# Optimization experiments

Hardware: AMD Instinct MI355X
Metric: run time of the kernel (lower is better)

Reference implementation:

```python
import jax, jax.numpy as jnp
import numpy as np

Z, Y, X = 200, 8, 200
XM, YM, ZM = 80.0, 6.0, 80.0  # x_meter, y_meter, z_meter
IMG_H, IMG_W = 256, 512
FEAT_C, OUT_CH = 64, 128
EPS = 1e-8


def create_grid3d():
    # matches torch create_grid3d flattening order (z, y, x), x/y shifted by -0.5
    zz, yy, xx = jnp.meshgrid(jnp.linspace(0.0, 1.0, Z),
                              jnp.linspace(0.0, 1.0, Y),
                              jnp.linspace(0.0, 1.0, X), indexing='ij')
    xyz = jnp.stack([xx.ravel() - 0.5, yy.ravel() - 0.5, zz.ravel()], axis=1)  # (N,3)
    return xyz * jnp.array([XM, YM, ZM], dtype=jnp.float32)


def setup_inputs() -> dict:
    key = jax.random.key(0)
    k1, k2, k3 = jax.random.split(key, 3)
    B = 2
    img_feat = jax.random.normal(k1, (B, FEAT_C, 32, 64), dtype=jnp.float32)
    # realistic pinhole intrinsics so many voxels project in-bounds
    K = jnp.array([[300.0, 0.0, IMG_W / 2.0],
                   [0.0, 300.0, IMG_H / 2.0],
                   [0.0, 0.0, 1.0]], dtype=jnp.float32)
    pix_T_cam = jnp.tile(K[None], (B, 1, 1))
    conv_w = jax.random.normal(k2, (OUT_CH, FEAT_C * Y), dtype=jnp.float32) * 0.02
    conv_b = jax.random.normal(k3, (OUT_CH,), dtype=jnp.float32) * 0.02
    return {"img_feat": img_feat, "pix_T_cam": pix_T_cam, "conv_w": conv_w, "conv_b": conv_b}


def reference(img_feat, pix_T_cam, conv_w, conv_b):
    B, C, H, W = img_feat.shape
    xyz = create_grid3d()  # (N,3), N = Z*Y*X
    pix = jnp.einsum('bij,nj->bni', pix_T_cam, xyz)  # (B,N,3)
    d = pix[..., 2]
    u01 = pix[..., 0] / (d + EPS) / IMG_W  # normalized [0,1] u
    v01 = pix[..., 1] / (d + EPS) / IMG_H
    valid = (u01 >= 0) & (v01 >= 0) & (u01 <= 1) & (v01 <= 1)  # (B,N)

    # grid_sample, align_corners=False, padding_mode='zeros' (D=1 collapses to bilinear)
    gx = u01 * 2.0 - 1.0
    gy = v01 * 2.0 - 1.0
    xp = ((gx + 1.0) * W - 1.0) * 0.5
    yp = ((gy + 1.0) * H - 1.0) * 0.5
    x0f = jnp.floor(xp); y0f = jnp.floor(yp)
    wx1 = xp - x0f; wy1 = yp - y0f
    x0 = x0f.astype(jnp.int32); y0 = y0f.astype(jnp.int32)
    bidx = jnp.arange(B)[:, None]

    def gather(xi, yi):
        ok = (xi >= 0) & (xi < W) & (yi >= 0) & (yi < H)
        xc = jnp.clip(xi, 0, W - 1)
        yc = jnp.clip(yi, 0, H - 1)
        vals = img_feat[bidx, :, yc, xc]  # (B,N,C)
        return vals * ok[..., None].astype(img_feat.dtype)

    v00 = gather(x0, y0)
    v01_ = gather(x0 + 1, y0)
    v10 = gather(x0, y0 + 1)
    v11 = gather(x0 + 1, y0 + 1)
    samp = (v00 * ((1 - wx1) * (1 - wy1))[..., None]
            + v01_ * (wx1 * (1 - wy1))[..., None]
            + v10 * ((1 - wx1) * wy1)[..., None]
            + v11 * (wx1 * wy1)[..., None])  # (B,N,C)
    samp = samp * valid[..., None].astype(samp.dtype)

    bev = samp.reshape(B, Z, Y, X, C)
    # rearrange 'b c d h w -> b (c h) d w' with d=Z, h=Y, w=X
    bev = jnp.transpose(bev, (0, 4, 2, 1, 3)).reshape(B, C * Y, Z, X)
    out = jnp.einsum('bczx,oc->bozx', bev, conv_w) + conv_b[None, :, None, None]
    return out
```

## Files before the change

### kernel.cpp

```cpp
#include <hip/hip_runtime.h>


#define NPOS 40000

typedef short bf16x8 __attribute__((ext_vector_type(8)));
typedef float f32x4  __attribute__((ext_vector_type(4)));

__device__ __forceinline__ unsigned rne16(float f) {
    unsigned u = __float_as_uint(f);
    return (u + 0x7fffu + ((u >> 16) & 1u)) >> 16;
}
__device__ __forceinline__ float lo16(unsigned u) { return __uint_as_float(u << 16); }
__device__ __forceinline__ float hi16(unsigned u) { return __uint_as_float(u & 0xffff0000u); }
__device__ __forceinline__ unsigned cvtpk(float lo, float hi) {
    unsigned r;
    asm("v_cvt_pk_bf16_f32 %0, %1, %2" : "=v"(r) : "v"(lo), "v"(hi));
    return r;
}
__device__ __forceinline__ void pkfma(float2& a, float2 v, float2 w) {
    asm("v_pk_fma_f32 %0, %1, %2, %0" : "+v"(a) : "v"(v), "v"(w));
}
__device__ __forceinline__ void tile_barrier() {
    asm volatile("s_waitcnt lgkmcnt(0)" ::: "memory");
    __builtin_amdgcn_s_barrier();
    __builtin_amdgcn_sched_barrier(0);
}

__global__ __launch_bounds__(256)
void bili_prep(const float* __restrict__ img, const float* __restrict__ convw,
               unsigned short* __restrict__ imgT, unsigned short* __restrict__ Wp)
{
    const int t = threadIdx.x;
    if (blockIdx.x < 128) {
        const int u   = blockIdx.x * 256 + t;
        const int li8 = u & 7, x = (u >> 3) & 63, y = (u >> 9) & 31, b = u >> 14;
        const float* src = img + (((b * 64 + li8 * 8) * 32 + y) * 64 + x);
        unsigned pk[4];
        #pragma unroll
        for (int cc = 0; cc < 8; ++cc) {
            const unsigned v = rne16(src[cc * 2048]);
            if ((cc & 1) == 0) pk[cc >> 1] = v;
            else               pk[cc >> 1] |= (v << 16);
        }
        ((uint4*)imgT)[u] = make_uint4(pk[0], pk[1], pk[2], pk[3]);
    } else {
        const int j = (blockIdx.x - 128) * 256 + t;
        const int k = j & 511, o = j >> 9;
        const int y = k >> 6, c = k & 63;
        Wp[j] = (unsigned short)rne16(convw[o * 512 + c * 8 + y]);
    }
}

__global__ __launch_bounds__(256, 3)
void bili_main(const char* __restrict__ imgTbytes,
               const unsigned short* __restrict__ Wp,
               const float* __restrict__ pixT,
               const float* __restrict__ convb,
               float* __restrict__ out)
{
    __shared__ uint4  Fb[2][1024];
    __shared__ uint4  offsB[512];
    __shared__ float4 wtsL[512];

    const int t   = threadIdx.x;
    const int bx  = blockIdx.x;
    const int b   = (bx >= 625) ? 1 : 0;
    const int n0  = (bx - b * 625) * 64;

    const int wv  = t >> 6;
    const int ln  = t & 63;
    const int l15 = ln & 15;
    const int lg  = ln >> 4;
    const int g   = t >> 3;
    const unsigned liOff = (unsigned)((t & 7) << 4);

    f32x4 acc0[4], acc1[4];
    {
        float bias0[4], bias1[4];
        #pragma unroll
        for (int r = 0; r < 4; ++r) {
            bias0[r] = convb[wv * 32 +      lg * 4 + r];
            bias1[r] = convb[wv * 32 + 16 + lg * 4 + r];
        }
        #pragma unroll
        for (int nt = 0; nt < 4; ++nt)
            #pragma unroll
            for (int r = 0; r < 4; ++r) { acc0[nt][r] = bias0[r]; acc1[nt][r] = bias1[r]; }
    }

    {
        const float* Kb = pixT + b * 9;
        const float K00 = Kb[0], K01 = Kb[1], K02 = Kb[2];
        const float K10 = Kb[3], K11 = Kb[4], K12 = Kb[5];
        const float K20 = Kb[6], K21 = Kb[7], K22 = Kb[8];

        #pragma unroll
        for (int r = 0; r < 2; ++r) {
            const int p    = r * 256 + t;
            const int nloc = p >> 3;
            const int y    = p & 7;
            const int n = n0 + nloc;
            const int z = n / 200;
            const int x = n - z * 200;

            const float pxv = (x * (1.0f / 199.0f) - 0.5f) * 80.0f;
            const float pzv = (z * (1.0f / 199.0f)) * 80.0f;
            const float pyv = (y * (1.0f / 7.0f) - 0.5f) * 6.0f;

            const float p0 = K00 * pxv + K01 * pyv + K02 * pzv;
            const float p1 = K10 * pxv + K11 * pyv + K12 * pzv;
            const float d  = K20 * pxv + K21 * pyv + K22 * pzv;
            const float inv = __builtin_amdgcn_rcpf(d + 1e-8f);
            const float u01 = p0 * inv * (1.0f / 512.0f);
            const float v01 = p1 * inv * (1.0f / 256.0f);
            const float vf = (u01 >= 0.0f && u01 <= 1.0f &&
                              v01 >= 0.0f && v01 <= 1.0f) ? 1.0f : 0.0f;

            float xp = u01 * 64.0f - 0.5f;
            xp = fminf(fmaxf(xp, -2.0f), 66.0f);
            const float x0f = floorf(xp);
            const float wx = xp - x0f;
            const int x0 = (int)x0f, x1i = x0 + 1;
            const float wx0 = (1.0f - wx) * vf * ((x0  >= 0 && x0  < 64) ? 1.0f : 0.0f);
            const float wx1 = wx          * vf * ((x1i >= 0 && x1i < 64) ? 1.0f : 0.0f);
            const int xi0 = min(max(x0, 0), 63);
            const int xi1 = min(max(x1i, 0), 63);

            float yp = v01 * 32.0f - 0.5f;
            yp = fminf(fmaxf(yp, -2.0f), 34.0f);
            const float y0f = floorf(yp);
            const float wy = yp - y0f;
            const int y0 = (int)y0f, y1i = y0 + 1;
            const float wy0 = (1.0f - wy) * ((y0  >= 0 && y0  < 32) ? 1.0f : 0.0f);
            const float wy1 = wy          * ((y1i >= 0 && y1i < 32) ? 1.0f : 0.0f);
            const int yi0 = min(max(y0, 0), 31);
            const int yi1 = min(max(y1i, 0), 31);

            const unsigned o0 = (unsigned)(((yi0 << 6) + xi0) << 7);
            const unsigned o1 = (unsigned)(((yi0 << 6) + xi1) << 7);
            const unsigned o2 = (unsigned)(((yi1 << 6) + xi0) << 7);
            const unsigned o3 = (unsigned)(((yi1 << 6) + xi1) << 7);

            wtsL[p]  = make_float4(wx0 * wy0, wx1 * wy0, wx0 * wy1, wx1 * wy1);
            offsB[p] = make_uint4(o0, o1, o2, o3);
        }
    }

    tile_barrier();

    const char*   imgTb = imgTbytes + (size_t)b * 262144;
    const bf16x8* ApG   = (const bf16x8*)Wp;
    const bf16x8* Ap0   = ApG + ((wv * 32 +      l15) * 64 + lg);
    const bf16x8* Ap1   = ApG + ((wv * 32 + 16 + l15) * 64 + lg);

    uint4 sbE[8], sbO[8];

    #define ISSUE_H(q, hb, SB)                                                 \
        _Pragma("unroll")                                                      \
        for (int it2 = 0; it2 < 2; ++it2) {                                    \
            const int pp = ((hb) * 2 + it2) * 32 + g;                          \
            const int n_ = pp >> 1, ys = pp & 1;                               \
            const int p_ = n_ * 8 + 2 * (q) + ys;                              \
            const uint4 oc = offsB[p_];                                        \
            SB[it2 * 4 + 0] = *(const uint4*)(imgTb + (size_t)(oc.x | liOff)); \
            SB[it2 * 4 + 1] = *(const uint4*)(imgTb + (size_t)(oc.y | liOff)); \
            SB[it2 * 4 + 2] = *(const uint4*)(imgTb + (size_t)(oc.z | liOff)); \
            SB[it2 * 4 + 3] = *(const uint4*)(imgTb + (size_t)(oc.w | liOff)); \
        }

    #define PROC_H(q, hb, SB, buf)                                             \
        _Pragma("unroll")                                                      \
        for (int it2 = 0; it2 < 2; ++it2) {                                    \
            const int pp = ((hb) * 2 + it2) * 32 + g;                          \
            const int n_ = pp >> 1, ys = pp & 1;                               \
            const int p_ = n_ * 8 + 2 * (q) + ys;                              \
            const float4 w = wtsL[p_];                                         \
            float2 ac[4];                                                      \
            _Pragma("unroll")                                                  \
            for (int qq = 0; qq < 4; ++qq) ac[qq] = make_float2(0.0f, 0.0f);   \
            _Pragma("unroll")                                                  \
            for (int j = 0; j < 4; ++j) {                                      \
                const uint4 v = SB[it2 * 4 + j];                               \
                const float ww = (j == 0) ? w.x : (j == 1) ? w.y : (j == 2) ? w.z : w.w; \
                const float2 w2 = make_float2(ww, ww);                         \
                float2 t0, t1, t2, t3;                                         \
                t0.x = lo16(v.x); t0.y = hi16(v.x);                            \
                t1.x = lo16(v.y); t1.y = hi16(v.y);                            \
                t2.x = lo16(v.z); t2.y = hi16(v.z);                            \
                t3.x = lo16(v.w); t3.y = hi16(v.w);                            \
                pkfma(ac[0], t0, w2);                                          \
                pkfma(ac[1], t1, w2);                                          \
                pkfma(ac[2], t2, w2);                                          \
                pkfma(ac[3], t3, w2);                                          \
            }                                                                  \
            uint4 pk;                                                          \
            pk.x = cvtpk(ac[0].x, ac[0].y);                                    \
            pk.y = cvtpk(ac[1].x, ac[1].y);                                    \
            pk.z = cvtpk(ac[2].x, ac[2].y);                                    \
            pk.w = cvtpk(ac[3].x, ac[3].y);                                    \
            (buf)[n_ * 16 + ((ys * 8 + (t & 7)) ^ (n_ & 7))] = pk;             \
        }

    #define MFMA_H(q, hf, buf)                                                 \
        do {                                                                   \
            const bf16x8* Fv = (const bf16x8*)(buf);                           \
            __builtin_amdgcn_s_setprio(1);                                     \
            _Pragma("unroll")                                                  \
            for (int k2 = 0; k2 < 2; ++k2) {                                   \
                const int k = (hf) * 2 + k2;                                   \
                const bf16x8 a0_ = Ap0[((q) * 4 + k) * 4];                     \
                const bf16x8 a1_ = Ap1[((q) * 4 + k) * 4];                     \
                _Pragma("unroll")                                              \
                for (int nt = 0; nt < 4; ++nt) {                               \
                    const int nn = nt * 16 + l15;                              \
                    const bf16x8 bv = Fv[nn * 16 + ((k * 4 + lg) ^ (nn & 7))]; \
                    acc0[nt] = __builtin_amdgcn_mfma_f32_16x16x32_bf16(a0_, bv, acc0[nt], 0, 0, 0); \
                    acc1[nt] = __builtin_amdgcn_mfma_f32_16x16x32_bf16(a1_, bv, acc1[nt], 0, 0, 0); \
                }                                                              \
            }                                                                  \
            __builtin_amdgcn_s_setprio(0);                                     \
        } while (0)

    ISSUE_H(0, 0, sbE);
    ISSUE_H(0, 1, sbO);
    PROC_H (0, 0, sbE, Fb[0]);
    ISSUE_H(1, 0, sbE);
    PROC_H (0, 1, sbO, Fb[0]);
    tile_barrier();

    ISSUE_H(1, 1, sbO);
    MFMA_H (0, 0, Fb[0]);
    PROC_H (1, 0, sbE, Fb[1]);
    ISSUE_H(2, 0, sbE);
    MFMA_H (0, 1, Fb[0]);
    PROC_H (1, 1, sbO, Fb[1]);
    tile_barrier();

    ISSUE_H(2, 1, sbO);
    MFMA_H (1, 0, Fb[1]);
    PROC_H (2, 0, sbE, Fb[0]);
    ISSUE_H(3, 0, sbE);
    MFMA_H (1, 1, Fb[1]);
    PROC_H (2, 1, sbO, Fb[0]);
    tile_barrier();

    ISSUE_H(3, 1, sbO);
    MFMA_H (2, 0, Fb[0]);
    PROC_H (3, 0, sbE, Fb[1]);
    MFMA_H (2, 1, Fb[0]);
    PROC_H (3, 1, sbO, Fb[1]);
    tile_barrier();

    MFMA_H (3, 0, Fb[1]);
    MFMA_H (3, 1, Fb[1]);

    #undef ISSUE_H
    #undef PROC_H
    #undef MFMA_H

    {
        float* ob = out + (size_t)(b * 128 + wv * 32) * NPOS + n0;
        #pragma unroll
        for (int nt = 0; nt < 4; ++nt) {
            #pragma unroll
            for (int r = 0; r < 4; ++r) {
                ob[(     lg * 4 + r) * NPOS + nt * 16 + l15] = acc0[nt][r];
                ob[(16 + lg * 4 + r) * NPOS + nt * 16 + l15] = acc1[nt][r];
            }
        }
    }
}

extern "C" void kernel_launch(void* const* d_in, const int* in_sizes, int n_in,
                              void* d_out, int out_size, void* d_ws, size_t ws_size,
                              hipStream_t stream) {
    const float* img   = (const float*)d_in[0];
    const float* pixT  = (const float*)d_in[1];
    const float* convw = (const float*)d_in[2];
    const float* convb = (const float*)d_in[3];
    float* out = (float*)d_out;

    unsigned short* imgT = (unsigned short*)d_ws;
    unsigned short* Wp   = imgT + 262144;

    hipLaunchKernelGGL(bili_prep, dim3(384), dim3(256), 0, stream,
                       img, convw, imgT, Wp);
    hipLaunchKernelGGL(bili_main, dim3(1250), dim3(256), 0, stream,
                       (const char*)imgT, Wp, pixT, convb, out);
}
```

Before: 48.44 us.

## Double block size to 512 threads, one 16-channel MFMA tile per wave, preload weights

The main kernel now launches 512 threads per block (8 waves) instead of 256. Each wave owns 16 output channels instead of 32, and each thread computes one sample point and gathers one sample group per stage instead of two. The wave's bf16 weight fragments for the whole K dimension are preloaded into 16 registers up front instead of being read from global memory inside the MFMA loop. This spreads the gather and blend work over more waves and cuts per-thread serial work and weight reload latency, at the cost of more register pressure and larger block barriers.

New measurement: 54.69 us. 1.13x slower.

```diff
diff --git a/kernel.cpp b/kernel.cpp
--- a/kernel.cpp
+++ b/kernel.cpp
@@ -51,7 +51,7 @@
     }
 }
 
-__global__ __launch_bounds__(256, 3)
+__global__ __launch_bounds__(512, 3)
 void bili_main(const char* __restrict__ imgTbytes,
                const unsigned short* __restrict__ Wp,
                const float* __restrict__ pixT,
@@ -74,18 +74,21 @@
     const int g   = t >> 3;
     const unsigned liOff = (unsigned)((t & 7) << 4);
 
-    f32x4 acc0[4], acc1[4];
-    {
-        float bias0[4], bias1[4];
-        #pragma unroll
-        for (int r = 0; r < 4; ++r) {
-            bias0[r] = convb[wv * 32 +      lg * 4 + r];
-            bias1[r] = convb[wv * 32 + 16 + lg * 4 + r];
+    const bf16x8* ApG = (const bf16x8*)Wp;
+    bf16x8 wA[16];
+    {
+        const bf16x8* Ap = ApG + ((wv * 16 + l15) * 64 + lg);
+        #pragma unroll
+        for (int ks = 0; ks < 16; ++ks) wA[ks] = Ap[ks * 4];
+    }
+    f32x4 acc[4];
+    {
+        const float4 bv = *(const float4*)(convb + wv * 16 + lg * 4);
+        #pragma unroll
+        for (int nt = 0; nt < 4; ++nt) {
+            acc[nt][0] = bv.x; acc[nt][1] = bv.y;
+            acc[nt][2] = bv.z; acc[nt][3] = bv.w;
         }
-        #pragma unroll
-        for (int nt = 0; nt < 4; ++nt)
-            #pragma unroll
-            for (int r = 0; r < 4; ++r) { acc0[nt][r] = bias0[r]; acc1[nt][r] = bias1[r]; }
     }
 
     {
@@ -94,84 +97,75 @@
         const float K10 = Kb[3], K11 = Kb[4], K12 = Kb[5];
         const float K20 = Kb[6], K21 = Kb[7], K22 = Kb[8];
 
-        #pragma unroll
-        for (int r = 0; r < 2; ++r) {
-            const int p    = r * 256 + t;
-            const int nloc = p >> 3;
-            const int y    = p & 7;
-            const int n = n0 + nloc;
-            const int z = n / 200;
-            const int x = n - z * 200;
-
-            const float pxv = (x * (1.0f / 199.0f) - 0.5f) * 80.0f;
-            const float pzv = (z * (1.0f / 199.0f)) * 80.0f;
-            const float pyv = (y * (1.0f / 7.0f) - 0.5f) * 6.0f;
-
-            const float p0 = K00 * pxv + K01 * pyv + K02 * pzv;
-            const float p1 = K10 * pxv + K11 * pyv + K12 * pzv;
-            const float d  = K20 * pxv + K21 * pyv + K22 * pzv;
-            const float inv = __builtin_amdgcn_rcpf(d + 1e-8f);
-            const float u01 = p0 * inv * (1.0f / 512.0f);
-            const float v01 = p1 * inv * (1.0f / 256.0f);
-            const float vf = (u01 >= 0.0f && u01 <= 1.0f &&
-                              v01 >= 0.0f && v01 <= 1.0f) ? 1.0f : 0.0f;
-
-            float xp = u01 * 64.0f - 0.5f;
-            xp = fminf(fmaxf(xp, -2.0f), 66.0f);
-            const float x0f = floorf(xp);
-            const float wx = xp - x0f;
-            const int x0 = (int)x0f, x1i = x0 + 1;
-            const float wx0 = (1.0f - wx) * vf * ((x0  >= 0 && x0  < 64) ? 1.0f : 0.0f);
-            const float wx1 = wx          * vf * ((x1i >= 0 && x1i < 64) ? 1.0f : 0.0f);
-            const int xi0 = min(max(x0, 0), 63);
-            const int xi1 = min(max(x1i, 0), 63);
-
-            float yp = v01 * 32.0f - 0.5f;
-            yp = fminf(fmaxf(yp, -2.0f), 34.0f);
-            const float y0f = floorf(yp);
-            const float wy = yp - y0f;
-            const int y0 = (int)y0f, y1i = y0 + 1;
-            const float wy0 = (1.0f - wy) * ((y0  >= 0 && y0  < 32) ? 1.0f : 0.0f);
-            const float wy1 = wy          * ((y1i >= 0 && y1i < 32) ? 1.0f : 0.0f);
-            const int yi0 = min(max(y0, 0), 31);
-            const int yi1 = min(max(y1i, 0), 31);
-
-            const unsigned o0 = (unsigned)(((yi0 << 6) + xi0) << 7);
-            const unsigned o1 = (unsigned)(((yi0 << 6) + xi1) << 7);
-            const unsigned o2 = (unsigned)(((yi1 << 6) + xi0) << 7);
-            const unsigned o3 = (unsigned)(((yi1 << 6) + xi1) << 7);
-
-            wtsL[p]  = make_float4(wx0 * wy0, wx1 * wy0, wx0 * wy1, wx1 * wy1);
-            offsB[p] = make_uint4(o0, o1, o2, o3);
-        }
-    }
-
-    tile_barrier();
-
-    const char*   imgTb = imgTbytes + (size_t)b * 262144;
-    const bf16x8* ApG   = (const bf16x8*)Wp;
-    const bf16x8* Ap0   = ApG + ((wv * 32 +      l15) * 64 + lg);
-    const bf16x8* Ap1   = ApG + ((wv * 32 + 16 + l15) * 64 + lg);
-
-    uint4 sbE[8], sbO[8];
+        const int p    = t;
+        const int nloc = p >> 3;
+        const int y    = p & 7;
+        const int n = n0 + nloc;
+        const int z = n / 200;
+        const int x = n - z * 200;
+
+        const float pxv = (x * (1.0f / 199.0f) - 0.5f) * 80.0f;
+        const float pzv = (z * (1.0f / 199.0f)) * 80.0f;
+        const float pyv = (y * (1.0f / 7.0f) - 0.5f) * 6.0f;
+
+        const float p0 = K00 * pxv + K01 * pyv + K02 * pzv;
+        const float p1 = K10 * pxv + K11 * pyv + K12 * pzv;
+        const float d  = K20 * pxv + K21 * pyv + K22 * pzv;
+        const float inv = __builtin_amdgcn_rcpf(d + 1e-8f);
+        const float u01 = p0 * inv * (1.0f / 512.0f);
+        const float v01 = p1 * inv * (1.0f / 256.0f);
+        const float vf = (u01 >= 0.0f && u01 <= 1.0f &&
+                          v01 >= 0.0f && v01 <= 1.0f) ? 1.0f : 0.0f;
+
+        float xp = u01 * 64.0f - 0.5f;
+        xp = fminf(fmaxf(xp, -2.0f), 66.0f);
+        const float x0f = floorf(xp);
+        const float wx = xp - x0f;
+        const int x0 = (int)x0f, x1i = x0 + 1;
+        const float wx0 = (1.0f - wx) * vf * ((x0  >= 0 && x0  < 64) ? 1.0f : 0.0f);
+        const float wx1 = wx          * vf * ((x1i >= 0 && x1i < 64) ? 1.0f : 0.0f);
+        const int xi0 = min(max(x0, 0), 63);
+        const int xi1 = min(max(x1i, 0), 63);
+
+        float yp = v01 * 32.0f - 0.5f;
+        yp = fminf(fmaxf(yp, -2.0f), 34.0f);
+        const float y0f = floorf(yp);
+        const float wy = yp - y0f;
+        const int y0 = (int)y0f, y1i = y0 + 1;
+        const float wy0 = (1.0f - wy) * ((y0  >= 0 && y0  < 32) ? 1.0f : 0.0f);
+        const float wy1 = wy          * ((y1i >= 0 && y1i < 32) ? 1.0f : 0.0f);
+        const int yi0 = min(max(y0, 0), 31);
+        const int yi1 = min(max(y1i, 0), 31);
+
+        const unsigned o0 = (unsigned)(((yi0 << 6) + xi0) << 7);
+        const unsigned o1 = (unsigned)(((yi0 << 6) + xi1) << 7);
+        const unsigned o2 = (unsigned)(((yi1 << 6) + xi0) << 7);
+        const unsigned o3 = (unsigned)(((yi1 << 6) + xi1) << 7);
+
+        wtsL[p]  = make_float4(wx0 * wy0, wx1 * wy0, wx0 * wy1, wx1 * wy1);
+        offsB[p] = make_uint4(o0, o1, o2, o3);
+    }
+
+    tile_barrier();
+
+    const char* imgTb = imgTbytes + (size_t)b * 262144;
+    uint4 sbE[4], sbO[4];
 
     #define ISSUE_H(q, hb, SB)                                                 \
-        _Pragma("unroll")                                                      \
-        for (int it2 = 0; it2 < 2; ++it2) {                                    \
-            const int pp = ((hb) * 2 + it2) * 32 + g;                          \
+        do {                                                                   \
+            const int pp = (hb) * 64 + g;                                      \
             const int n_ = pp >> 1, ys = pp & 1;                               \
             const int p_ = n_ * 8 + 2 * (q) + ys;                              \
             const uint4 oc = offsB[p_];                                        \
-            SB[it2 * 4 + 0] = *(const uint4*)(imgTb + (size_t)(oc.x | liOff)); \
-            SB[it2 * 4 + 1] = *(const uint4*)(imgTb + (size_t)(oc.y | liOff)); \
-            SB[it2 * 4 + 2] = *(const uint4*)(imgTb + (size_t)(oc.z | liOff)); \
-            SB[it2 * 4 + 3] = *(const uint4*)(imgTb + (size_t)(oc.w | liOff)); \
-        }
+            SB[0] = *(const uint4*)(imgTb + (size_t)(oc.x | liOff));           \
+            SB[1] = *(const uint4*)(imgTb + (size_t)(oc.y | liOff));           \
+            SB[2] = *(const uint4*)(imgTb + (size_t)(oc.z | liOff));           \
+            SB[3] = *(const uint4*)(imgTb + (size_t)(oc.w | liOff));           \
+        } while (0)
 
     #define PROC_H(q, hb, SB, buf)                                             \
-        _Pragma("unroll")                                                      \
-        for (int it2 = 0; it2 < 2; ++it2) {                                    \
-            const int pp = ((hb) * 2 + it2) * 32 + g;                          \
+        do {                                                                   \
+            const int pp = (hb) * 64 + g;                                      \
             const int n_ = pp >> 1, ys = pp & 1;                               \
             const int p_ = n_ * 8 + 2 * (q) + ys;                              \
             const float4 w = wtsL[p_];                                         \
@@ -180,7 +174,7 @@
             for (int qq = 0; qq < 4; ++qq) ac[qq] = make_float2(0.0f, 0.0f);   \
             _Pragma("unroll")                                                  \
             for (int j = 0; j < 4; ++j) {                                      \
-                const uint4 v = SB[it2 * 4 + j];                               \
+                const uint4 v = SB[j];                                         \
                 const float ww = (j == 0) ? w.x : (j == 1) ? w.y : (j == 2) ? w.z : w.w; \
                 const float2 w2 = make_float2(ww, ww);                         \
                 float2 t0, t1, t2, t3;                                         \
@@ -199,7 +193,7 @@
             pk.z = cvtpk(ac[2].x, ac[2].y);                                    \
             pk.w = cvtpk(ac[3].x, ac[3].y);                                    \
             (buf)[n_ * 16 + ((ys * 8 + (t & 7)) ^ (n_ & 7))] = pk;             \
-        }
+        } while (0)
 
     #define MFMA_H(q, hf, buf)                                                 \
         do {                                                                   \
@@ -208,14 +202,12 @@
             _Pragma("unroll")                                                  \
             for (int k2 = 0; k2 < 2; ++k2) {                                   \
                 const int k = (hf) * 2 + k2;                                   \
-                const bf16x8 a0_ = Ap0[((q) * 4 + k) * 4];                     \
-                const bf16x8 a1_ = Ap1[((q) * 4 + k) * 4];                     \
+                const bf16x8 a_ = wA[(q) * 4 + k];                             \
                 _Pragma("unroll")                                              \
                 for (int nt = 0; nt < 4; ++nt) {                               \
                     const int nn = nt * 16 + l15;                              \
                     const bf16x8 bv = Fv[nn * 16 + ((k * 4 + lg) ^ (nn & 7))]; \
-                    acc0[nt] = __builtin_amdgcn_mfma_f32_16x16x32_bf16(a0_, bv, acc0[nt], 0, 0, 0); \
-                    acc1[nt] = __builtin_amdgcn_mfma_f32_16x16x32_bf16(a1_, bv, acc1[nt], 0, 0, 0); \
+                    acc[nt] = __builtin_amdgcn_mfma_f32_16x16x32_bf16(a_, bv, acc[nt], 0, 0, 0); \
                 }                                                              \
             }                                                                  \
             __builtin_amdgcn_s_setprio(0);                                     \
@@ -259,13 +251,12 @@
     #undef MFMA_H
 
     {
-        float* ob = out + (size_t)(b * 128 + wv * 32) * NPOS + n0;
+        float* ob = out + (size_t)(b * 128 + wv * 16) * NPOS + n0;
         #pragma unroll
         for (int nt = 0; nt < 4; ++nt) {
             #pragma unroll
             for (int r = 0; r < 4; ++r) {
-                ob[(     lg * 4 + r) * NPOS + nt * 16 + l15] = acc0[nt][r];
-                ob[(16 + lg * 4 + r) * NPOS + nt * 16 + l15] = acc1[nt][r];
+                ob[(lg * 4 + r) * NPOS + nt * 16 + l15] = acc[nt][r];
             }
         }
     }
@@ -285,6 +276,6 @@
 
     hipLaunchKernelGGL(bili_prep, dim3(384), dim3(256), 0, stream,
                        img, convw, imgT, Wp);
-    hipLaunchKernelGGL(bili_main, dim3(1250), dim3(256), 0, stream,
+    hipLaunchKernelGGL(bili_main, dim3(1250), dim3(512), 0, stream,
                        (const char*)imgT, Wp, pixT, convb, out);
 }
```
